# Optimization experiments

Hardware: AMD Instinct MI355X
Metric: run time of the kernel (lower is better)

## Reference

```python
import jax, jax.numpy as jnp
import numpy as np

B, N, C, R = 8, 1024, 256, 16


def setup_inputs() -> dict:
    key = jax.random.key(0)
    kq, kk, kwq, kwk, kbq, kbk, kr = jax.random.split(key, 7)
    init = 0.02
    return {
        "query_states": jax.random.normal(kq, (B, N, C), dtype=jnp.float32),
        "key_states": jax.random.normal(kk, (B, N, C), dtype=jnp.float32),
        "W_q": jax.random.normal(kwq, (C, C), dtype=jnp.float32) * init,
        "b_q": jax.random.normal(kbq, (C,), dtype=jnp.float32) * init,
        "W_k": jax.random.normal(kwk, (C, C), dtype=jnp.float32) * init,
        "b_k": jax.random.normal(kbk, (C,), dtype=jnp.float32) * init,
        "R_map": jax.random.normal(kr, (N, N, R), dtype=jnp.float32),
    }


def reference(query_states, key_states, W_q, b_q, W_k, b_k, R_map):
    input_dtype = query_states.dtype
    c = query_states.shape[-1]
    # Q/K linear projections (torch Linear: x @ W.T + b)
    qh = query_states @ W_q.T + b_q  # (B, N, C)
    kh = key_states @ W_k.T + b_k    # (B, N, C)
    # batched QK^T score in fp32 (original casts to float32 before bmm)
    scores = jnp.einsum(
        "bic,bjc->bij", qh.astype(jnp.float32), kh.astype(jnp.float32)
    ) / jnp.sqrt(jnp.asarray(c, jnp.float32))  # (B, N, N)
    # elementwise relation-mask multiply: broadcast over relation axis
    rel_mask = jnp.transpose(R_map, (2, 0, 1))  # (R, N, N)
    relation = scores[:, None, :, :] * rel_mask[None]  # (B, R, N, N)
    return relation.astype(input_dtype)
```

## Files before the change

### kernel.cpp

```cpp
#include <hip/hip_runtime.h>
#include <hip/hip_bf16.h>


typedef float  floatx4 __attribute__((ext_vector_type(4)));
typedef short  shortx8 __attribute__((ext_vector_type(8)));

__device__ __forceinline__ short f2bf(float f) {
    unsigned int u = __builtin_bit_cast(unsigned int, f);
    u += 0x7fffu + ((u >> 16) & 1u);
    return (short)(u >> 16);
}

__global__ __launch_bounds__(64) void proj_kernel(
    const float* __restrict__ Xq, const float* __restrict__ Wq, const float* __restrict__ bq,
    const float* __restrict__ Xk, const float* __restrict__ Wk, const float* __restrict__ bk,
    short* __restrict__ qh, short* __restrict__ kh)
{
    const float* X; const float* W; const float* bias; short* outp;
    if (blockIdx.z == 0) { X = Xq; W = Wq; bias = bq; outp = qh; }
    else                 { X = Xk; W = Wk; bias = bk; outp = kh; }

    const int lane  = threadIdx.x;
    const int row16 = lane & 15;
    const int quad  = lane >> 4;
    const int m0 = blockIdx.x * 16;
    const int c0 = blockIdx.y * 64;

    const float* xr = X + (size_t)(m0 + row16) * 256 + quad * 8;
    const float* wr = W + (size_t)(c0 + row16) * 256 + quad * 8;

    floatx4 acc[4];
#pragma unroll
    for (int nt = 0; nt < 4; nt++) acc[nt] = floatx4{0.f, 0.f, 0.f, 0.f};

#pragma unroll
    for (int k = 0; k < 256; k += 32) {
        float4 a0 = *(const float4*)(xr + k);
        float4 a1 = *(const float4*)(xr + k + 4);
        shortx8 af = { f2bf(a0.x), f2bf(a0.y), f2bf(a0.z), f2bf(a0.w),
                       f2bf(a1.x), f2bf(a1.y), f2bf(a1.z), f2bf(a1.w) };
#pragma unroll
        for (int nt = 0; nt < 4; nt++) {
            const float* w0 = wr + (size_t)nt * 16 * 256 + k;
            float4 b0 = *(const float4*)(w0);
            float4 b1 = *(const float4*)(w0 + 4);
            shortx8 bf = { f2bf(b0.x), f2bf(b0.y), f2bf(b0.z), f2bf(b0.w),
                           f2bf(b1.x), f2bf(b1.y), f2bf(b1.z), f2bf(b1.w) };
            acc[nt] = __builtin_amdgcn_mfma_f32_16x16x32_bf16(af, bf, acc[nt], 0, 0, 0);
        }
    }

#pragma unroll
    for (int nt = 0; nt < 4; nt++) {
        const int c = c0 + nt * 16 + row16;
        const float bv = bias[c];
#pragma unroll
        for (int r = 0; r < 4; r++) {
            const int m = m0 + quad * 4 + r;
            outp[(size_t)m * 256 + c] = f2bf(acc[nt][r] + bv);
        }
    }
}

__global__ __launch_bounds__(256) void score_mul_kernel(
    const short* __restrict__ qh, const short* __restrict__ kh,
    const float* __restrict__ Rm, float* __restrict__ out)
{
    const int lin  = blockIdx.x + 8 * (blockIdx.y + 16 * blockIdx.z);
    const int b    = (lin >> 3) & 7;
    const int tile = (lin & 7) + ((lin >> 6) << 3);
    const int j0 = (tile & 15) * 64;
    const int i0 = (tile >> 4) * 64;

    const int tid   = threadIdx.x;
    const int wave  = tid >> 6;
    const int lane  = tid & 63;
    const int row16 = lane & 15;
    const int quad  = lane >> 4;

    __shared__ float s_lds[64 * 68];

    const short* qbase = qh + ((size_t)(b * 1024 + i0 + wave * 16 + row16)) * 256 + quad * 8;
    const short* kbase = kh + ((size_t)(b * 1024 + j0 + row16)) * 256 + quad * 8;

    floatx4 acc[4];
#pragma unroll
    for (int nt = 0; nt < 4; nt++) acc[nt] = floatx4{0.f, 0.f, 0.f, 0.f};

#pragma unroll
    for (int k = 0; k < 256; k += 32) {
        shortx8 af = *(const shortx8*)(qbase + k);
#pragma unroll
        for (int nt = 0; nt < 4; nt++) {
            shortx8 bf = *(const shortx8*)(kbase + (size_t)nt * 16 * 256 + k);
            acc[nt] = __builtin_amdgcn_mfma_f32_16x16x32_bf16(af, bf, acc[nt], 0, 0, 0);
        }
    }

    const float inv = 0.0625f;
#pragma unroll
    for (int nt = 0; nt < 4; nt++) {
#pragma unroll
        for (int r = 0; r < 4; r++) {
            const int il = wave * 16 + quad * 4 + r;
            const int jl = nt * 16 + row16;
            s_lds[il * 68 + jl] = acc[nt][r] * inv;
        }
    }
    __syncthreads();

    const int j4 = lane & 15;
    const int rg = lane >> 4;
    const int w  = tid >> 6;
    const size_t NN = (size_t)1024 * 1024;

    float* ob = out + ((size_t)(b * 16 + rg * 4)) * NN + j0 + j4 * 4;

#pragma unroll 2
    for (int ii = 0; ii < 16; ii++) {
        const int il = w * 16 + ii;
        const int i  = i0 + il;
        floatx4 s4 = *(const floatx4*)&s_lds[il * 68 + j4 * 4];
        const float* rp = Rm + ((size_t)i * 1024 + j0 + j4 * 4) * 16 + rg * 4;
        floatx4 q0 = *(const floatx4*)(rp);
        floatx4 q1 = *(const floatx4*)(rp + 16);
        floatx4 q2 = *(const floatx4*)(rp + 32);
        floatx4 q3 = *(const floatx4*)(rp + 48);
        float* op = ob + (size_t)i * 1024;

        floatx4 v0 = { s4[0] * q0[0], s4[1] * q1[0], s4[2] * q2[0], s4[3] * q3[0] };
        __builtin_nontemporal_store(v0, (floatx4*)(op));
        floatx4 v1 = { s4[0] * q0[1], s4[1] * q1[1], s4[2] * q2[1], s4[3] * q3[1] };
        __builtin_nontemporal_store(v1, (floatx4*)(op + NN));
        floatx4 v2 = { s4[0] * q0[2], s4[1] * q1[2], s4[2] * q2[2], s4[3] * q3[2] };
        __builtin_nontemporal_store(v2, (floatx4*)(op + 2 * NN));
        floatx4 v3 = { s4[0] * q0[3], s4[1] * q1[3], s4[2] * q2[3], s4[3] * q3[3] };
        __builtin_nontemporal_store(v3, (floatx4*)(op + 3 * NN));
    }
}

extern "C" void kernel_launch(void* const* d_in, const int* in_sizes, int n_in,
                              void* d_out, int out_size, void* d_ws, size_t ws_size,
                              hipStream_t stream) {
    const float* q   = (const float*)d_in[0];
    const float* k   = (const float*)d_in[1];
    const float* Wq  = (const float*)d_in[2];
    const float* bq  = (const float*)d_in[3];
    const float* Wk  = (const float*)d_in[4];
    const float* bk  = (const float*)d_in[5];
    const float* Rm  = (const float*)d_in[6];
    float* out = (float*)d_out;

    short* qh = (short*)d_ws;
    short* kh = (short*)d_ws + (size_t)8192 * 256;

    dim3 pgrid(512, 4, 2);
    proj_kernel<<<pgrid, 64, 0, stream>>>(q, Wq, bq, k, Wk, bk, qh, kh);

    dim3 sgrid(8, 16, 16);
    score_mul_kernel<<<sgrid, 256, 0, stream>>>(qh, kh, Rm, out);
}
```

Baseline: 683.4 us.

## Retile score kernel to full 16-row stripes with per-thread 16-relation writes

```diff
diff --git a/kernel.cpp b/kernel.cpp
--- a/kernel.cpp
+++ b/kernel.cpp
@@ -66,76 +66,65 @@
     const short* __restrict__ qh, const short* __restrict__ kh,
     const float* __restrict__ Rm, float* __restrict__ out)
 {
-    const int lin  = blockIdx.x + 8 * (blockIdx.y + 16 * blockIdx.z);
-    const int b    = (lin >> 3) & 7;
-    const int tile = (lin & 7) + ((lin >> 6) << 3);
-    const int j0 = (tile & 15) * 64;
-    const int i0 = (tile >> 4) * 64;
+    const int itile = blockIdx.x;
+    const int b     = blockIdx.y;
+    const int i0    = itile * 16;
 
     const int tid   = threadIdx.x;
-    const int wave  = tid >> 6;
+    const int w     = tid >> 6;
     const int lane  = tid & 63;
     const int row16 = lane & 15;
     const int quad  = lane >> 4;
 
-    __shared__ float s_lds[64 * 68];
+    __shared__ float s_lds[16 * 1024];
 
-    const short* qbase = qh + ((size_t)(b * 1024 + i0 + wave * 16 + row16)) * 256 + quad * 8;
-    const short* kbase = kh + ((size_t)(b * 1024 + j0 + row16)) * 256 + quad * 8;
+    const short* qbase = qh + ((size_t)(b * 1024 + i0 + row16)) * 256 + quad * 8;
+    shortx8 a[8];
+#pragma unroll
+    for (int ks = 0; ks < 8; ks++) a[ks] = *(const shortx8*)(qbase + ks * 32);
 
-    floatx4 acc[4];
+    const short* kb = kh + ((size_t)(b * 1024 + w * 256 + row16)) * 256 + quad * 8;
+    const float inv = 0.0625f;
+
+#pragma unroll 2
+    for (int jt = 0; jt < 16; jt++) {
+        floatx4 acc = {0.f, 0.f, 0.f, 0.f};
+        const short* kr = kb + (size_t)jt * 16 * 256;
 #pragma unroll
-    for (int nt = 0; nt < 4; nt++) acc[nt] = floatx4{0.f, 0.f, 0.f, 0.f};
-
+        for (int ks = 0; ks < 8; ks++) {
+            shortx8 bfr = *(const shortx8*)(kr + ks * 32);
+            acc = __builtin_amdgcn_mfma_f32_16x16x32_bf16(a[ks], bfr, acc, 0, 0, 0);
+        }
 #pragma unroll
-    for (int k = 0; k < 256; k += 32) {
-        shortx8 af = *(const shortx8*)(qbase + k);
-#pragma unroll
-        for (int nt = 0; nt < 4; nt++) {
-            shortx8 bf = *(const shortx8*)(kbase + (size_t)nt * 16 * 256 + k);
-            acc[nt] = __builtin_amdgcn_mfma_f32_16x16x32_bf16(af, bf, acc[nt], 0, 0, 0);
-        }
-    }
-
-    const float inv = 0.0625f;
-#pragma unroll
-    for (int nt = 0; nt < 4; nt++) {
-#pragma unroll
-        for (int r = 0; r < 4; r++) {
-            const int il = wave * 16 + quad * 4 + r;
-            const int jl = nt * 16 + row16;
-            s_lds[il * 68 + jl] = acc[nt][r] * inv;
-        }
+        for (int r = 0; r < 4; r++)
+            s_lds[(quad * 4 + r) * 1024 + w * 256 + jt * 16 + row16] = acc[r] * inv;
     }
     __syncthreads();
 
-    const int j4 = lane & 15;
-    const int rg = lane >> 4;
-    const int w  = tid >> 6;
+    const int jc = w * 256 + lane * 4;
     const size_t NN = (size_t)1024 * 1024;
+    float* ob = out + (size_t)(b * 16) * NN + jc;
 
-    float* ob = out + ((size_t)(b * 16 + rg * 4)) * NN + j0 + j4 * 4;
+    for (int il = 0; il < 16; il++) {
+        const int i = i0 + il;
+        floatx4 s4 = *(const floatx4*)&s_lds[il * 1024 + jc];
+        const float* rp = Rm + ((size_t)i * 1024 + jc) * 16;
 
-#pragma unroll 2
-    for (int ii = 0; ii < 16; ii++) {
-        const int il = w * 16 + ii;
-        const int i  = i0 + il;
-        floatx4 s4 = *(const floatx4*)&s_lds[il * 68 + j4 * 4];
-        const float* rp = Rm + ((size_t)i * 1024 + j0 + j4 * 4) * 16 + rg * 4;
-        floatx4 q0 = *(const floatx4*)(rp);
-        floatx4 q1 = *(const floatx4*)(rp + 16);
-        floatx4 q2 = *(const floatx4*)(rp + 32);
-        floatx4 q3 = *(const floatx4*)(rp + 48);
+        floatx4 q[4][4];
+#pragma unroll
+        for (int jo = 0; jo < 4; jo++)
+#pragma unroll
+            for (int rg = 0; rg < 4; rg++)
+                q[jo][rg] = *(const floatx4*)(rp + jo * 16 + rg * 4);
+
         float* op = ob + (size_t)i * 1024;
-
-        floatx4 v0 = { s4[0] * q0[0], s4[1] * q1[0], s4[2] * q2[0], s4[3] * q3[0] };
-        __builtin_nontemporal_store(v0, (floatx4*)(op));
-        floatx4 v1 = { s4[0] * q0[1], s4[1] * q1[1], s4[2] * q2[1], s4[3] * q3[1] };
-        __builtin_nontemporal_store(v1, (floatx4*)(op + NN));
-        floatx4 v2 = { s4[0] * q0[2], s4[1] * q1[2], s4[2] * q2[2], s4[3] * q3[2] };
-        __builtin_nontemporal_store(v2, (floatx4*)(op + 2 * NN));
-        floatx4 v3 = { s4[0] * q0[3], s4[1] * q1[3], s4[2] * q2[3], s4[3] * q3[3] };
-        __builtin_nontemporal_store(v3, (floatx4*)(op + 3 * NN));
+#pragma unroll
+        for (int r = 0; r < 16; r++) {
+            const int rg = r >> 2, rs = r & 3;
+            floatx4 v = { q[0][rg][rs] * s4[0], q[1][rg][rs] * s4[1],
+                          q[2][rg][rs] * s4[2], q[3][rg][rs] * s4[3] };
+            __builtin_nontemporal_store(v, (floatx4*)(op + (size_t)r * NN));
+        }
     }
 }
 
@@ -157,6 +146,6 @@
     dim3 pgrid(512, 4, 2);
     proj_kernel<<<pgrid, 64, 0, stream>>>(q, Wq, bq, k, Wk, bk, qh, kh);
 
-    dim3 sgrid(8, 16, 16);
+    dim3 sgrid(64, 8);
     score_mul_kernel<<<sgrid, 256, 0, stream>>>(qh, kh, Rm, out);
 }
```

Result: faster. 668.1 us (-2.2%).
